# Kernel tuning notes

Hardware: AMD Instinct MI355X
Metric: run time of the kernel (lower is better)

## Reference

```python
import jax, jax.numpy as jnp
import numpy as np

D_MODEL = 1024
NUM_HEAD = 16
D_K = D_MODEL // NUM_HEAD


def setup_inputs() -> dict:
    key = jax.random.key(0)
    ks = jax.random.split(key, 11)
    B, S = 2, 2048
    s = 1.0 / np.sqrt(D_MODEL)
    return {
        "q": jax.random.normal(ks[0], (B, S, D_MODEL), jnp.float32),
        "k": jax.random.normal(ks[1], (B, S, D_MODEL), jnp.float32),
        "v": jax.random.normal(ks[2], (B, S, D_MODEL), jnp.float32),
        "Wq": jax.random.normal(ks[3], (D_MODEL, D_MODEL), jnp.float32) * s,
        "bq": jnp.zeros((D_MODEL,), jnp.float32),
        "Wk": jax.random.normal(ks[4], (D_MODEL, D_MODEL), jnp.float32) * s,
        "bk": jnp.zeros((D_MODEL,), jnp.float32),
        "Wv": jax.random.normal(ks[5], (D_MODEL, D_MODEL), jnp.float32) * s,
        "bv": jnp.zeros((D_MODEL,), jnp.float32),
        "Wo": jax.random.normal(ks[6], (D_MODEL, D_MODEL), jnp.float32) * s,
        "bo": jnp.zeros((D_MODEL,), jnp.float32),
    }


def _split_head(x, B):
    # [B, S, d_model] -> [B, H, S, d_k]
    S = x.shape[1]
    return x.reshape(B, S, NUM_HEAD, D_K).transpose(0, 2, 1, 3)


def reference(q, k, v, Wq, bq, Wk, bk, Wv, bv, Wo, bo):
    B = q.shape[0]
    qh = _split_head(q @ Wq + bq, B)  # [B,H,Sq,dk]
    kh = _split_head(k @ Wk + bk, B)  # [B,H,Sk,dk]
    vh = _split_head(v @ Wv + bv, B)  # [B,H,Sk,dk]
    scores = jnp.einsum("bhqd,bhkd->bhqk", qh, kh) / jnp.sqrt(
        jnp.asarray(D_K, qh.dtype)
    )
    attn = jax.nn.softmax(scores, axis=-1)
    out = jnp.einsum("bhqk,bhkd->bhqd", attn, vh)  # [B,H,Sq,dk]
    out = out.transpose(0, 2, 1, 3).reshape(B, -1, D_MODEL)
    return jax.nn.relu(out @ Wo + bo)
```

## Files before the change

### kernel.cpp

```cpp
#include <hip/hip_runtime.h>
#include <math.h>

#define SEQ 2048
#define NHD 16

typedef float f32x4 __attribute__((ext_vector_type(4), may_alias));
typedef _Float16 h16x8 __attribute__((ext_vector_type(8), may_alias));
typedef _Float16 h16x4 __attribute__((ext_vector_type(4), may_alias));

__device__ __forceinline__ void gl_lds16(const void* g, void* l) {
  __builtin_amdgcn_global_load_lds(
      (const __attribute__((address_space(1))) unsigned int*)g,
      (__attribute__((address_space(3))) unsigned int*)l, 16, 0, 0);
}

struct PrepArgs {
  const float* W[4];
  _Float16* T[4];
  const float* X[3];
  _Float16* H[3];
};

__global__ __launch_bounds__(256) void prep_k(PrepArgs a) {
  __shared__ float tile[64][65];
  const int blk = blockIdx.x;
  const int t = threadIdx.x;
  if (blk < 1024) {
    const int widx = blk >> 8, tl = blk & 255;
    const int nb = (tl & 15) * 64, kb = (tl >> 4) * 64;
    const float* __restrict__ W = a.W[widx];
    _Float16* __restrict__ T = a.T[widx];
    const int c = t & 63, r0 = t >> 6;
#pragma unroll
    for (int i = 0; i < 16; ++i) {
      const int r = i * 4 + r0;
      tile[r][c] = W[(size_t)(kb + r) * 1024 + nb + c];
    }
    __syncthreads();
#pragma unroll
    for (int i = 0; i < 16; ++i) {
      const int n = i * 4 + r0;
      T[(size_t)(nb + n) * 1024 + kb + c] = (_Float16)tile[c][n];
    }
  } else {
    const int b2 = blk - 1024;
    const int z = b2 >> 11, bx = b2 & 2047;
    const float* __restrict__ X = a.X[z];
    _Float16* __restrict__ H = a.H[z];
    const size_t i = ((size_t)bx * 256 + t) * 8;
    const f32x4 f0 = *(const f32x4*)(X + i);
    const f32x4 f1 = *(const f32x4*)(X + i + 4);
    const float fs[8] = {f0.x, f0.y, f0.z, f0.w, f1.x, f1.y, f1.z, f1.w};
    h16x8 o;
#pragma unroll
    for (int j = 0; j < 8; ++j) o[j] = (_Float16)fs[j];
    *(h16x8*)(H + i) = o;
  }
}

__global__ __launch_bounds__(256) void vtrans_k(const unsigned short* __restrict__ Vb,
                                                unsigned short* __restrict__ Vt) {
  __shared__ unsigned short tile[64][65];
  const int t = threadIdx.x;
  const int c = t & 63, r0 = t >> 6;
  const int s0 = blockIdx.x * 64;
  const int bh = blockIdx.y;
#pragma unroll
  for (int i = 0; i < 16; ++i) {
    const int r = i * 4 + r0;
    tile[r][c] = Vb[((size_t)bh * SEQ + s0 + r) * 64 + c];
  }
  __syncthreads();
#pragma unroll
  for (int i = 0; i < 16; ++i) {
    const int d = i * 4 + r0;
    const int sp = ((c & 15) * 4) + (c >> 4);
    Vt[((size_t)bh * 64 + d) * SEQ + s0 + sp] = tile[c][d];
  }
}

struct QKVArgs {
  const _Float16* A[3];
  const _Float16* Bt[3];
  const float* bias[3];
  _Float16* C[3];
};

__global__ __launch_bounds__(256, 4) void gemm_qkv_k(QKVArgs a) {
  __shared__ char smem[16384];
  h16x8* lds8 = (h16x8*)smem;
  const int z = blockIdx.z;
  const _Float16* __restrict__ A = a.A[z];
  const _Float16* __restrict__ Bt = a.Bt[z];
  const float* __restrict__ bias = a.bias[z];
  _Float16* __restrict__ C = a.C[z];

  const int t = threadIdx.x;
  const int l = t & 63, w = t >> 6;
  const int quad = l >> 4, l15 = l & 15;
  const int wm = w >> 1, wn = w & 1;
  const int n0 = blockIdx.x * 128, m0 = blockIdx.y * 128;

  const f32x4 z4 = {0.f, 0.f, 0.f, 0.f};
  f32x4 acc[4][4];
#pragma unroll
  for (int i = 0; i < 4; ++i)
#pragma unroll
    for (int j = 0; j < 4; ++j) acc[i][j] = z4;

  for (int k0 = 0; k0 < 1024; k0 += 32) {
#pragma unroll
    for (int it = 0; it < 2; ++it) {
      const int c = it * 4 + w;
      const int rr = c * 16 + l15;
      gl_lds16(A + (size_t)(m0 + rr) * 1024 + k0 + quad * 8, smem + c * 1024);
      gl_lds16(Bt + (size_t)(n0 + rr) * 1024 + k0 + quad * 8, smem + 8192 + c * 1024);
    }
    __syncthreads();
    h16x8 af[4], bf[4];
#pragma unroll
    for (int i = 0; i < 4; ++i) {
      af[i] = lds8[(wm * 4 + i) * 64 + l];
      bf[i] = lds8[512 + (wn * 4 + i) * 64 + l];
    }
#pragma unroll
    for (int i = 0; i < 4; ++i)
#pragma unroll
      for (int j = 0; j < 4; ++j)
        acc[i][j] = __builtin_amdgcn_mfma_f32_16x16x32_f16(af[i], bf[j], acc[i][j], 0, 0, 0);
    __syncthreads();
  }
#pragma unroll
  for (int i = 0; i < 4; ++i)
#pragma unroll
    for (int j = 0; j < 4; ++j) {
      const int col = n0 + wn * 64 + j * 16 + l15;
      const float bv = bias[col];
#pragma unroll
      for (int r = 0; r < 4; ++r) {
        const int row = m0 + wm * 64 + i * 16 + quad * 4 + r;
        const int b = row >> 11, s = row & 2047;
        const int h = col >> 6, d = col & 63;
        C[((size_t)(b * NHD + h) * SEQ + s) * 64 + d] = (_Float16)(acc[i][j][r] + bv);
      }
    }
}

__global__ __launch_bounds__(256, 4) void gemm_o_k(
    const _Float16* __restrict__ A, const _Float16* __restrict__ Bt,
    const float* __restrict__ bias, float* __restrict__ Cf) {
  __shared__ char smem[16384];
  h16x8* lds8 = (h16x8*)smem;
  const int t = threadIdx.x;
  const int l = t & 63, w = t >> 6;
  const int quad = l >> 4, l15 = l & 15;
  const int wm = w >> 1, wn = w & 1;
  const int n0 = blockIdx.x * 128, m0 = blockIdx.y * 128;

  const f32x4 z4 = {0.f, 0.f, 0.f, 0.f};
  f32x4 acc[4][4];
#pragma unroll
  for (int i = 0; i < 4; ++i)
#pragma unroll
    for (int j = 0; j < 4; ++j) acc[i][j] = z4;

  for (int k0 = 0; k0 < 1024; k0 += 32) {
#pragma unroll
    for (int it = 0; it < 2; ++it) {
      const int c = it * 4 + w;
      const int rr = c * 16 + l15;
      gl_lds16(A + (size_t)(m0 + rr) * 1024 + k0 + quad * 8, smem + c * 1024);
      gl_lds16(Bt + (size_t)(n0 + rr) * 1024 + k0 + quad * 8, smem + 8192 + c * 1024);
    }
    __syncthreads();
    h16x8 af[4], bf[4];
#pragma unroll
    for (int i = 0; i < 4; ++i) {
      af[i] = lds8[(wm * 4 + i) * 64 + l];
      bf[i] = lds8[512 + (wn * 4 + i) * 64 + l];
    }
#pragma unroll
    for (int i = 0; i < 4; ++i)
#pragma unroll
      for (int j = 0; j < 4; ++j)
        acc[i][j] = __builtin_amdgcn_mfma_f32_16x16x32_f16(af[i], bf[j], acc[i][j], 0, 0, 0);
    __syncthreads();
  }
#pragma unroll
  for (int i = 0; i < 4; ++i)
#pragma unroll
    for (int j = 0; j < 4; ++j) {
      const int col = n0 + wn * 64 + j * 16 + l15;
      const float bv = bias[col];
#pragma unroll
      for (int r = 0; r < 4; ++r) {
        const int row = m0 + wm * 64 + i * 16 + quad * 4 + r;
        Cf[(size_t)row * 1024 + col] = fmaxf(acc[i][j][r] + bv, 0.f);
      }
    }
}

__global__ __launch_bounds__(256, 4) void attn_k(
    const _Float16* __restrict__ Qf, const _Float16* __restrict__ Kf,
    const _Float16* __restrict__ Vtp, _Float16* __restrict__ Of) {
  __shared__ char smem[34816];
  h16x8* lds8 = (h16x8*)smem;
  const int t = threadIdx.x;
  const int l = t & 63, w = t >> 6;
  const int quad = l >> 4, l15 = l & 15;
  const int q0 = blockIdx.x * 128;
  const int bh = blockIdx.y;
  const int b = bh >> 4, h = bh & 15;

  const _Float16* Kb = Kf + (size_t)bh * SEQ * 64;
  const _Float16* Vtb = Vtp + (size_t)bh * 64 * SEQ;

  h16x8 qf[2][2];
#pragma unroll
  for (int mi = 0; mi < 2; ++mi) {
    const size_t qb = ((size_t)bh * SEQ + q0 + w * 32 + mi * 16 + l15) * 64;
#pragma unroll
    for (int ks = 0; ks < 2; ++ks)
      qf[mi][ks] = *(const h16x8*)&Qf[qb + ks * 32 + quad * 8];
  }
  const f32x4 z4 = {0.f, 0.f, 0.f, 0.f};
  f32x4 oacc[2][4], lacc[2];
#pragma unroll
  for (int mi = 0; mi < 2; ++mi) {
    lacc[mi] = z4;
#pragma unroll
    for (int i = 0; i < 4; ++i) oacc[mi][i] = z4;
  }
  h16x8 ones;
#pragma unroll
  for (int j = 0; j < 8; ++j) ones[j] = (_Float16)1.0f;

  for (int k0 = 0; k0 < SEQ; k0 += 64) {
#pragma unroll
    for (int it = 0; it < 2; ++it) {
      const int c = it * 4 + w;
      const int kd = (c >> 1) * 16 + l15;
      const int off2 = (c & 1) * 32 + quad * 8;
      gl_lds16(Kb + (size_t)(k0 + kd) * 64 + off2, smem + c * 1024);
      gl_lds16(Vtb + (size_t)kd * SEQ + k0 + off2, smem + 8192 + c * 1024);
    }
    __syncthreads();

    {
      h16x8 kfr[4][2];
#pragma unroll
      for (int nt = 0; nt < 4; ++nt)
#pragma unroll
        for (int ks = 0; ks < 2; ++ks) kfr[nt][ks] = lds8[(nt * 2 + ks) * 64 + l];

#pragma unroll
      for (int mi = 0; mi < 2; ++mi) {
        f32x4 sacc[4];
#pragma unroll
        for (int nt = 0; nt < 4; ++nt) {
          f32x4 s = z4;
          s = __builtin_amdgcn_mfma_f32_16x16x32_f16(qf[mi][0], kfr[nt][0], s, 0, 0, 0);
          s = __builtin_amdgcn_mfma_f32_16x16x32_f16(qf[mi][1], kfr[nt][1], s, 0, 0, 0);
          sacc[nt] = s;
        }
        char* pb = smem + 16384 + (w * 2 + mi) * 2304;
#pragma unroll
        for (int r = 0; r < 4; ++r) {
          h16x4 pk;
#pragma unroll
          for (int nt = 0; nt < 4; ++nt)
            pk[nt] = (_Float16)__expf(sacc[nt][r] * 0.125f);
          *(h16x4*)(pb + (quad * 4 + r) * 144 + l15 * 8) = pk;
        }
      }
    }
    __asm__ __volatile__("" ::: "memory");

    {
      h16x8 vfr[4][2];
#pragma unroll
      for (int nt = 0; nt < 4; ++nt)
#pragma unroll
        for (int ks = 0; ks < 2; ++ks) vfr[nt][ks] = lds8[512 + (nt * 2 + ks) * 64 + l];

#pragma unroll
      for (int mi = 0; mi < 2; ++mi) {
        char* pb = smem + 16384 + (w * 2 + mi) * 2304;
        const h16x8 pf0 = *(const h16x8*)(pb + l15 * 144 + quad * 16);
        const h16x8 pf1 = *(const h16x8*)(pb + l15 * 144 + 64 + quad * 16);
        lacc[mi] = __builtin_amdgcn_mfma_f32_16x16x32_f16(pf0, ones, lacc[mi], 0, 0, 0);
        lacc[mi] = __builtin_amdgcn_mfma_f32_16x16x32_f16(pf1, ones, lacc[mi], 0, 0, 0);
#pragma unroll
        for (int nt = 0; nt < 4; ++nt) {
          oacc[mi][nt] = __builtin_amdgcn_mfma_f32_16x16x32_f16(pf0, vfr[nt][0], oacc[mi][nt], 0, 0, 0);
          oacc[mi][nt] = __builtin_amdgcn_mfma_f32_16x16x32_f16(pf1, vfr[nt][1], oacc[mi][nt], 0, 0, 0);
        }
      }
    }
    __syncthreads();
  }

#pragma unroll
  for (int mi = 0; mi < 2; ++mi)
#pragma unroll
    for (int nt = 0; nt < 4; ++nt)
#pragma unroll
      for (int r = 0; r < 4; ++r) {
        const float o = oacc[mi][nt][r] / lacc[mi][r];
        const size_t tok = (size_t)b * SEQ + q0 + w * 32 + mi * 16 + quad * 4 + r;
        Of[tok * 1024 + h * 64 + nt * 16 + l15] = (_Float16)o;
      }
}

extern "C" void kernel_launch(void* const* d_in, const int* in_sizes, int n_in,
                              void* d_out, int out_size, void* d_ws, size_t ws_size,
                              hipStream_t stream) {
  const float* q = (const float*)d_in[0];
  const float* k = (const float*)d_in[1];
  const float* v = (const float*)d_in[2];
  const float* Wq = (const float*)d_in[3];
  const float* bq = (const float*)d_in[4];
  const float* Wk = (const float*)d_in[5];
  const float* bk = (const float*)d_in[6];
  const float* Wv = (const float*)d_in[7];
  const float* bv = (const float*)d_in[8];
  const float* Wo = (const float*)d_in[9];
  const float* bo = (const float*)d_in[10];

  char* W8 = (char*)d_ws;
  const size_t MB = 1024 * 1024;
  auto F = [&](size_t off) { return (_Float16*)(W8 + off); };
  _Float16* wt[4] = {F(0), F(2 * MB), F(4 * MB), F(6 * MB)};
  _Float16* qf = F(8 * MB);
  _Float16* kf = F(16 * MB);
  _Float16* vf = F(24 * MB);
  _Float16* Qf = F(32 * MB);
  _Float16* Kf = F(40 * MB);
  _Float16* Vb = F(48 * MB);
  _Float16* Vt = F(56 * MB);
  _Float16* Of = F(64 * MB);

  const dim3 blk(256);

  PrepArgs pa;
  pa.W[0] = Wq; pa.W[1] = Wk; pa.W[2] = Wv; pa.W[3] = Wo;
  pa.T[0] = wt[0]; pa.T[1] = wt[1]; pa.T[2] = wt[2]; pa.T[3] = wt[3];
  pa.X[0] = q; pa.X[1] = k; pa.X[2] = v;
  pa.H[0] = qf; pa.H[1] = kf; pa.H[2] = vf;
  prep_k<<<dim3(7168), blk, 0, stream>>>(pa);

  QKVArgs qa;
  qa.A[0] = qf; qa.A[1] = kf; qa.A[2] = vf;
  qa.Bt[0] = wt[0]; qa.Bt[1] = wt[1]; qa.Bt[2] = wt[2];
  qa.bias[0] = bq; qa.bias[1] = bk; qa.bias[2] = bv;
  qa.C[0] = Qf; qa.C[1] = Kf; qa.C[2] = Vb;
  gemm_qkv_k<<<dim3(8, 32, 3), blk, 0, stream>>>(qa);

  vtrans_k<<<dim3(32, 32), blk, 0, stream>>>((const unsigned short*)Vb,
                                             (unsigned short*)Vt);
  attn_k<<<dim3(16, 32), blk, 0, stream>>>(Qf, Kf, Vt, Of);
  gemm_o_k<<<dim3(8, 32), blk, 0, stream>>>(Of, wt[3], bo, (float*)d_out);
}
```

Before: 261.2 us.

## Split attention over key halves with combine pass; deepen GEMM K-step

Attention is split across two key-range halves through a third grid dimension, doubling the block count so more CUs are occupied. Each half writes unnormalized partial outputs and row sums, and a new combine kernel adds them and normalizes. The QKV and output GEMMs now stage a 64-wide K slice per barrier pair, halving synchronizations at the cost of twice the LDS and a lower occupancy hint. This adds an extra kernel launch plus fp16 partial-output traffic, and it reuses workspace regions (Vb for Op0, qf for Of).

```diff
diff --git a/kernel.cpp b/kernel.cpp
--- a/kernel.cpp
+++ b/kernel.cpp
@@ -86,8 +86,8 @@
   _Float16* C[3];
 };
 
-__global__ __launch_bounds__(256, 4) void gemm_qkv_k(QKVArgs a) {
-  __shared__ char smem[16384];
+__global__ __launch_bounds__(256, 3) void gemm_qkv_k(QKVArgs a) {
+  __shared__ char smem[32768];
   h16x8* lds8 = (h16x8*)smem;
   const int z = blockIdx.z;
   const _Float16* __restrict__ A = a.A[z];
@@ -108,26 +108,32 @@
 #pragma unroll
     for (int j = 0; j < 4; ++j) acc[i][j] = z4;
 
-  for (int k0 = 0; k0 < 1024; k0 += 32) {
-#pragma unroll
-    for (int it = 0; it < 2; ++it) {
-      const int c = it * 4 + w;
+  for (int k0 = 0; k0 < 1024; k0 += 64) {
+#pragma unroll
+    for (int it = 0; it < 4; ++it) {
+      const int c2 = it * 4 + w;
+      const int ks = c2 >> 3;
+      const int c = c2 & 7;
       const int rr = c * 16 + l15;
-      gl_lds16(A + (size_t)(m0 + rr) * 1024 + k0 + quad * 8, smem + c * 1024);
-      gl_lds16(Bt + (size_t)(n0 + rr) * 1024 + k0 + quad * 8, smem + 8192 + c * 1024);
-    }
-    __syncthreads();
-    h16x8 af[4], bf[4];
-#pragma unroll
-    for (int i = 0; i < 4; ++i) {
-      af[i] = lds8[(wm * 4 + i) * 64 + l];
-      bf[i] = lds8[512 + (wn * 4 + i) * 64 + l];
-    }
-#pragma unroll
-    for (int i = 0; i < 4; ++i)
-#pragma unroll
-      for (int j = 0; j < 4; ++j)
-        acc[i][j] = __builtin_amdgcn_mfma_f32_16x16x32_f16(af[i], bf[j], acc[i][j], 0, 0, 0);
+      const size_t ko = k0 + ks * 32 + quad * 8;
+      gl_lds16(A + (size_t)(m0 + rr) * 1024 + ko, smem + ks * 8192 + c * 1024);
+      gl_lds16(Bt + (size_t)(n0 + rr) * 1024 + ko, smem + 16384 + ks * 8192 + c * 1024);
+    }
+    __syncthreads();
+#pragma unroll
+    for (int ks = 0; ks < 2; ++ks) {
+      h16x8 af[4], bf[4];
+#pragma unroll
+      for (int i = 0; i < 4; ++i) {
+        af[i] = lds8[ks * 512 + (wm * 4 + i) * 64 + l];
+        bf[i] = lds8[1024 + ks * 512 + (wn * 4 + i) * 64 + l];
+      }
+#pragma unroll
+      for (int i = 0; i < 4; ++i)
+#pragma unroll
+        for (int j = 0; j < 4; ++j)
+          acc[i][j] = __builtin_amdgcn_mfma_f32_16x16x32_f16(af[i], bf[j], acc[i][j], 0, 0, 0);
+    }
     __syncthreads();
   }
 #pragma unroll
@@ -146,10 +152,10 @@
     }
 }
 
-__global__ __launch_bounds__(256, 4) void gemm_o_k(
+__global__ __launch_bounds__(256, 3) void gemm_o_k(
     const _Float16* __restrict__ A, const _Float16* __restrict__ Bt,
     const float* __restrict__ bias, float* __restrict__ Cf) {
-  __shared__ char smem[16384];
+  __shared__ char smem[32768];
   h16x8* lds8 = (h16x8*)smem;
   const int t = threadIdx.x;
   const int l = t & 63, w = t >> 6;
@@ -164,26 +170,32 @@
 #pragma unroll
     for (int j = 0; j < 4; ++j) acc[i][j] = z4;
 
-  for (int k0 = 0; k0 < 1024; k0 += 32) {
-#pragma unroll
-    for (int it = 0; it < 2; ++it) {
-      const int c = it * 4 + w;
+  for (int k0 = 0; k0 < 1024; k0 += 64) {
+#pragma unroll
+    for (int it = 0; it < 4; ++it) {
+      const int c2 = it * 4 + w;
+      const int ks = c2 >> 3;
+      const int c = c2 & 7;
       const int rr = c * 16 + l15;
-      gl_lds16(A + (size_t)(m0 + rr) * 1024 + k0 + quad * 8, smem + c * 1024);
-      gl_lds16(Bt + (size_t)(n0 + rr) * 1024 + k0 + quad * 8, smem + 8192 + c * 1024);
-    }
-    __syncthreads();
-    h16x8 af[4], bf[4];
-#pragma unroll
-    for (int i = 0; i < 4; ++i) {
-      af[i] = lds8[(wm * 4 + i) * 64 + l];
-      bf[i] = lds8[512 + (wn * 4 + i) * 64 + l];
-    }
-#pragma unroll
-    for (int i = 0; i < 4; ++i)
-#pragma unroll
-      for (int j = 0; j < 4; ++j)
-        acc[i][j] = __builtin_amdgcn_mfma_f32_16x16x32_f16(af[i], bf[j], acc[i][j], 0, 0, 0);
+      const size_t ko = k0 + ks * 32 + quad * 8;
+      gl_lds16(A + (size_t)(m0 + rr) * 1024 + ko, smem + ks * 8192 + c * 1024);
+      gl_lds16(Bt + (size_t)(n0 + rr) * 1024 + ko, smem + 16384 + ks * 8192 + c * 1024);
+    }
+    __syncthreads();
+#pragma unroll
+    for (int ks = 0; ks < 2; ++ks) {
+      h16x8 af[4], bf[4];
+#pragma unroll
+      for (int i = 0; i < 4; ++i) {
+        af[i] = lds8[ks * 512 + (wm * 4 + i) * 64 + l];
+        bf[i] = lds8[1024 + ks * 512 + (wn * 4 + i) * 64 + l];
+      }
+#pragma unroll
+      for (int i = 0; i < 4; ++i)
+#pragma unroll
+        for (int j = 0; j < 4; ++j)
+          acc[i][j] = __builtin_amdgcn_mfma_f32_16x16x32_f16(af[i], bf[j], acc[i][j], 0, 0, 0);
+    }
     __syncthreads();
   }
 #pragma unroll
@@ -202,7 +214,9 @@
 
 __global__ __launch_bounds__(256, 4) void attn_k(
     const _Float16* __restrict__ Qf, const _Float16* __restrict__ Kf,
-    const _Float16* __restrict__ Vtp, _Float16* __restrict__ Of) {
+    const _Float16* __restrict__ Vtp,
+    _Float16* __restrict__ Op0, _Float16* __restrict__ Op1,
+    float* __restrict__ Lp) {
   __shared__ char smem[34816];
   h16x8* lds8 = (h16x8*)smem;
   const int t = threadIdx.x;
@@ -210,6 +224,7 @@
   const int quad = l >> 4, l15 = l & 15;
   const int q0 = blockIdx.x * 128;
   const int bh = blockIdx.y;
+  const int kz = blockIdx.z;
   const int b = bh >> 4, h = bh & 15;
 
   const _Float16* Kb = Kf + (size_t)bh * SEQ * 64;
@@ -235,7 +250,8 @@
 #pragma unroll
   for (int j = 0; j < 8; ++j) ones[j] = (_Float16)1.0f;
 
-  for (int k0 = 0; k0 < SEQ; k0 += 64) {
+  const int kbeg = kz * 1024;
+  for (int k0 = kbeg; k0 < kbeg + 1024; k0 += 64) {
 #pragma unroll
     for (int it = 0; it < 2; ++it) {
       const int c = it * 4 + w;
@@ -300,16 +316,43 @@
     __syncthreads();
   }
 
+  _Float16* __restrict__ Op = kz ? Op1 : Op0;
 #pragma unroll
   for (int mi = 0; mi < 2; ++mi)
 #pragma unroll
     for (int nt = 0; nt < 4; ++nt)
 #pragma unroll
       for (int r = 0; r < 4; ++r) {
-        const float o = oacc[mi][nt][r] / lacc[mi][r];
         const size_t tok = (size_t)b * SEQ + q0 + w * 32 + mi * 16 + quad * 4 + r;
-        Of[tok * 1024 + h * 64 + nt * 16 + l15] = (_Float16)o;
-      }
+        Op[tok * 1024 + h * 64 + nt * 16 + l15] = (_Float16)oacc[mi][nt][r];
+      }
+  if (l15 == 0) {
+#pragma unroll
+    for (int mi = 0; mi < 2; ++mi)
+#pragma unroll
+      for (int r = 0; r < 4; ++r) {
+        const int row = q0 + w * 32 + mi * 16 + quad * 4 + r;
+        Lp[(size_t)kz * 65536 + bh * 2048 + row] = lacc[mi][r];
+      }
+  }
+}
+
+__global__ __launch_bounds__(256) void combine_k(
+    const _Float16* __restrict__ Op0, const _Float16* __restrict__ Op1,
+    const float* __restrict__ Lp, _Float16* __restrict__ Of) {
+  const size_t e = ((size_t)blockIdx.x * 256 + threadIdx.x) * 8;
+  const int tok = (int)(e >> 10);
+  const int h = (int)((e & 1023) >> 6);
+  const int b = tok >> 11, s = tok & 2047;
+  const int bh = b * NHD + h;
+  const float inv = 1.f / (Lp[(size_t)bh * 2048 + s] + Lp[65536 + (size_t)bh * 2048 + s]);
+  const h16x8 o1 = *(const h16x8*)(Op0 + e);
+  const h16x8 o2 = *(const h16x8*)(Op1 + e);
+  h16x8 o;
+#pragma unroll
+  for (int j = 0; j < 8; ++j)
+    o[j] = (_Float16)(((float)o1[j] + (float)o2[j]) * inv);
+  *(h16x8*)(Of + e) = o;
 }
 
 extern "C" void kernel_launch(void* const* d_in, const int* in_sizes, int n_in,
@@ -338,7 +381,10 @@
   _Float16* Kf = F(40 * MB);
   _Float16* Vb = F(48 * MB);
   _Float16* Vt = F(56 * MB);
-  _Float16* Of = F(64 * MB);
+  _Float16* Op0 = F(48 * MB);
+  _Float16* Op1 = F(64 * MB);
+  float* Lp = (float*)(W8 + 72 * MB);
+  _Float16* Of = F(8 * MB);
 
   const dim3 blk(256);
 
@@ -358,6 +404,7 @@
 
   vtrans_k<<<dim3(32, 32), blk, 0, stream>>>((const unsigned short*)Vb,
                                              (unsigned short*)Vt);
-  attn_k<<<dim3(16, 32), blk, 0, stream>>>(Qf, Kf, Vt, Of);
+  attn_k<<<dim3(16, 32, 2), blk, 0, stream>>>(Qf, Kf, Vt, Op0, Op1, Lp);
+  combine_k<<<dim3(2048), blk, 0, stream>>>(Op0, Op1, Lp, Of);
   gemm_o_k<<<dim3(8, 32), blk, 0, stream>>>(Of, wt[3], bo, (float*)d_out);
 }
```

After: 258.4 us. About the same (-1.1%).

## Fuse input fp16 conversion into QKV GEMM and split attention keys in two

Applied to the files above, without the earlier changes.

The separate fp32-to-fp16 conversion pass over q/k/v is removed. The QKV GEMM now loads fp32 activations, converts them in registers and stores them into LDS, which saves a full read/write round trip through memory. Attention is split over the key dimension into two halves, doubling the grid. Each half writes unnormalised partial outputs plus row sums, and the output GEMM combines and normalises them while staging its A operand. This adds extra partial-output traffic, and the combine is only correct if both halves use a consistent softmax offset.

```diff
diff --git a/kernel.cpp b/kernel.cpp
--- a/kernel.cpp
+++ b/kernel.cpp
@@ -17,44 +17,25 @@
 struct PrepArgs {
   const float* W[4];
   _Float16* T[4];
-  const float* X[3];
-  _Float16* H[3];
 };
 
 __global__ __launch_bounds__(256) void prep_k(PrepArgs a) {
   __shared__ float tile[64][65];
-  const int blk = blockIdx.x;
-  const int t = threadIdx.x;
-  if (blk < 1024) {
-    const int widx = blk >> 8, tl = blk & 255;
-    const int nb = (tl & 15) * 64, kb = (tl >> 4) * 64;
-    const float* __restrict__ W = a.W[widx];
-    _Float16* __restrict__ T = a.T[widx];
-    const int c = t & 63, r0 = t >> 6;
-#pragma unroll
-    for (int i = 0; i < 16; ++i) {
-      const int r = i * 4 + r0;
-      tile[r][c] = W[(size_t)(kb + r) * 1024 + nb + c];
-    }
-    __syncthreads();
-#pragma unroll
-    for (int i = 0; i < 16; ++i) {
-      const int n = i * 4 + r0;
-      T[(size_t)(nb + n) * 1024 + kb + c] = (_Float16)tile[c][n];
-    }
-  } else {
-    const int b2 = blk - 1024;
-    const int z = b2 >> 11, bx = b2 & 2047;
-    const float* __restrict__ X = a.X[z];
-    _Float16* __restrict__ H = a.H[z];
-    const size_t i = ((size_t)bx * 256 + t) * 8;
-    const f32x4 f0 = *(const f32x4*)(X + i);
-    const f32x4 f1 = *(const f32x4*)(X + i + 4);
-    const float fs[8] = {f0.x, f0.y, f0.z, f0.w, f1.x, f1.y, f1.z, f1.w};
-    h16x8 o;
-#pragma unroll
-    for (int j = 0; j < 8; ++j) o[j] = (_Float16)fs[j];
-    *(h16x8*)(H + i) = o;
+  const int t = threadIdx.x;
+  const int c = t & 63, r0 = t >> 6;
+  const int nb = blockIdx.x * 64, kb = blockIdx.y * 64;
+  const float* __restrict__ W = a.W[blockIdx.z];
+  _Float16* __restrict__ T = a.T[blockIdx.z];
+#pragma unroll
+  for (int i = 0; i < 16; ++i) {
+    const int r = i * 4 + r0;
+    tile[r][c] = W[(size_t)(kb + r) * 1024 + nb + c];
+  }
+  __syncthreads();
+#pragma unroll
+  for (int i = 0; i < 16; ++i) {
+    const int n = i * 4 + r0;
+    T[(size_t)(nb + n) * 1024 + kb + c] = (_Float16)tile[c][n];
   }
 }
 
@@ -80,7 +61,7 @@
 }
 
 struct QKVArgs {
-  const _Float16* A[3];
+  const float* Af[3];
   const _Float16* Bt[3];
   const float* bias[3];
   _Float16* C[3];
@@ -90,7 +71,7 @@
   __shared__ char smem[16384];
   h16x8* lds8 = (h16x8*)smem;
   const int z = blockIdx.z;
-  const _Float16* __restrict__ A = a.A[z];
+  const float* __restrict__ Af = a.Af[z];
   const _Float16* __restrict__ Bt = a.Bt[z];
   const float* __restrict__ bias = a.bias[z];
   _Float16* __restrict__ C = a.C[z];
@@ -113,8 +94,21 @@
     for (int it = 0; it < 2; ++it) {
       const int c = it * 4 + w;
       const int rr = c * 16 + l15;
-      gl_lds16(A + (size_t)(m0 + rr) * 1024 + k0 + quad * 8, smem + c * 1024);
       gl_lds16(Bt + (size_t)(n0 + rr) * 1024 + k0 + quad * 8, smem + 8192 + c * 1024);
+    }
+#pragma unroll
+    for (int it = 0; it < 2; ++it) {
+      const int row = it * 64 + (t >> 2);
+      const int aq = t & 3;
+      const int slot = (row >> 4) * 64 + aq * 16 + (row & 15);
+      const float* src = Af + (size_t)(m0 + row) * 1024 + k0 + aq * 8;
+      const f32x4 f0 = *(const f32x4*)src;
+      const f32x4 f1 = *(const f32x4*)(src + 4);
+      const float fs[8] = {f0.x, f0.y, f0.z, f0.w, f1.x, f1.y, f1.z, f1.w};
+      h16x8 hv;
+#pragma unroll
+      for (int j = 0; j < 8; ++j) hv[j] = (_Float16)fs[j];
+      lds8[slot] = hv;
     }
     __syncthreads();
     h16x8 af[4], bf[4];
@@ -147,16 +141,28 @@
 }
 
 __global__ __launch_bounds__(256, 4) void gemm_o_k(
-    const _Float16* __restrict__ A, const _Float16* __restrict__ Bt,
+    const _Float16* __restrict__ Op0, const _Float16* __restrict__ Op1,
+    const float* __restrict__ Lp, const _Float16* __restrict__ Bt,
     const float* __restrict__ bias, float* __restrict__ Cf) {
-  __shared__ char smem[16384];
+  __shared__ char smem[24576];
   h16x8* lds8 = (h16x8*)smem;
+  float* inv_lds = (float*)(smem + 16384);
   const int t = threadIdx.x;
   const int l = t & 63, w = t >> 6;
   const int quad = l >> 4, l15 = l & 15;
   const int wm = w >> 1, wn = w & 1;
   const int n0 = blockIdx.x * 128, m0 = blockIdx.y * 128;
 
+#pragma unroll
+  for (int e = t; e < 2048; e += 256) {
+    const int rl = e >> 4, hh = e & 15;
+    const int m = m0 + rl;
+    const int b = m >> 11, s = m & 2047;
+    const size_t li = (size_t)(b * NHD + hh) * 2048 + s;
+    inv_lds[e] = 1.f / (Lp[li] + Lp[65536 + li]);
+  }
+  __syncthreads();
+
   const f32x4 z4 = {0.f, 0.f, 0.f, 0.f};
   f32x4 acc[4][4];
 #pragma unroll
@@ -169,8 +175,23 @@
     for (int it = 0; it < 2; ++it) {
       const int c = it * 4 + w;
       const int rr = c * 16 + l15;
-      gl_lds16(A + (size_t)(m0 + rr) * 1024 + k0 + quad * 8, smem + c * 1024);
       gl_lds16(Bt + (size_t)(n0 + rr) * 1024 + k0 + quad * 8, smem + 8192 + c * 1024);
+    }
+    const int head = k0 >> 6;
+#pragma unroll
+    for (int it = 0; it < 2; ++it) {
+      const int row = it * 64 + (t >> 2);
+      const int aq = t & 3;
+      const int slot = (row >> 4) * 64 + aq * 16 + (row & 15);
+      const size_t off = (size_t)(m0 + row) * 1024 + k0 + aq * 8;
+      const h16x8 a0 = *(const h16x8*)(Op0 + off);
+      const h16x8 a1 = *(const h16x8*)(Op1 + off);
+      const float inv = inv_lds[row * 16 + head];
+      h16x8 hv;
+#pragma unroll
+      for (int j = 0; j < 8; ++j)
+        hv[j] = (_Float16)(((float)a0[j] + (float)a1[j]) * inv);
+      lds8[slot] = hv;
     }
     __syncthreads();
     h16x8 af[4], bf[4];
@@ -202,7 +223,9 @@
 
 __global__ __launch_bounds__(256, 4) void attn_k(
     const _Float16* __restrict__ Qf, const _Float16* __restrict__ Kf,
-    const _Float16* __restrict__ Vtp, _Float16* __restrict__ Of) {
+    const _Float16* __restrict__ Vtp,
+    _Float16* __restrict__ Op0, _Float16* __restrict__ Op1,
+    float* __restrict__ Lp) {
   __shared__ char smem[34816];
   h16x8* lds8 = (h16x8*)smem;
   const int t = threadIdx.x;
@@ -210,6 +233,7 @@
   const int quad = l >> 4, l15 = l & 15;
   const int q0 = blockIdx.x * 128;
   const int bh = blockIdx.y;
+  const int kz = blockIdx.z;
   const int b = bh >> 4, h = bh & 15;
 
   const _Float16* Kb = Kf + (size_t)bh * SEQ * 64;
@@ -235,7 +259,8 @@
 #pragma unroll
   for (int j = 0; j < 8; ++j) ones[j] = (_Float16)1.0f;
 
-  for (int k0 = 0; k0 < SEQ; k0 += 64) {
+  const int kbeg = kz * 1024;
+  for (int k0 = kbeg; k0 < kbeg + 1024; k0 += 64) {
 #pragma unroll
     for (int it = 0; it < 2; ++it) {
       const int c = it * 4 + w;
@@ -300,16 +325,25 @@
     __syncthreads();
   }
 
+  _Float16* __restrict__ Op = kz ? Op1 : Op0;
 #pragma unroll
   for (int mi = 0; mi < 2; ++mi)
 #pragma unroll
     for (int nt = 0; nt < 4; ++nt)
 #pragma unroll
       for (int r = 0; r < 4; ++r) {
-        const float o = oacc[mi][nt][r] / lacc[mi][r];
         const size_t tok = (size_t)b * SEQ + q0 + w * 32 + mi * 16 + quad * 4 + r;
-        Of[tok * 1024 + h * 64 + nt * 16 + l15] = (_Float16)o;
-      }
+        Op[tok * 1024 + h * 64 + nt * 16 + l15] = (_Float16)oacc[mi][nt][r];
+      }
+  if (l15 == 0) {
+#pragma unroll
+    for (int mi = 0; mi < 2; ++mi)
+#pragma unroll
+      for (int r = 0; r < 4; ++r) {
+        const int row = q0 + w * 32 + mi * 16 + quad * 4 + r;
+        Lp[(size_t)kz * 65536 + bh * 2048 + row] = lacc[mi][r];
+      }
+  }
 }
 
 extern "C" void kernel_launch(void* const* d_in, const int* in_sizes, int n_in,
@@ -331,26 +365,23 @@
   const size_t MB = 1024 * 1024;
   auto F = [&](size_t off) { return (_Float16*)(W8 + off); };
   _Float16* wt[4] = {F(0), F(2 * MB), F(4 * MB), F(6 * MB)};
-  _Float16* qf = F(8 * MB);
-  _Float16* kf = F(16 * MB);
-  _Float16* vf = F(24 * MB);
-  _Float16* Qf = F(32 * MB);
-  _Float16* Kf = F(40 * MB);
-  _Float16* Vb = F(48 * MB);
-  _Float16* Vt = F(56 * MB);
-  _Float16* Of = F(64 * MB);
+  _Float16* Vb = F(8 * MB);
+  _Float16* Vt = F(16 * MB);
+  _Float16* Qf = F(24 * MB);
+  _Float16* Kf = F(32 * MB);
+  _Float16* Op0 = F(40 * MB);
+  _Float16* Op1 = F(48 * MB);
+  float* Lp = (float*)(W8 + 56 * MB);
 
   const dim3 blk(256);
 
   PrepArgs pa;
   pa.W[0] = Wq; pa.W[1] = Wk; pa.W[2] = Wv; pa.W[3] = Wo;
   pa.T[0] = wt[0]; pa.T[1] = wt[1]; pa.T[2] = wt[2]; pa.T[3] = wt[3];
-  pa.X[0] = q; pa.X[1] = k; pa.X[2] = v;
-  pa.H[0] = qf; pa.H[1] = kf; pa.H[2] = vf;
-  prep_k<<<dim3(7168), blk, 0, stream>>>(pa);
+  prep_k<<<dim3(16, 16, 4), blk, 0, stream>>>(pa);
 
   QKVArgs qa;
-  qa.A[0] = qf; qa.A[1] = kf; qa.A[2] = vf;
+  qa.Af[0] = q; qa.Af[1] = k; qa.Af[2] = v;
   qa.Bt[0] = wt[0]; qa.Bt[1] = wt[1]; qa.Bt[2] = wt[2];
   qa.bias[0] = bq; qa.bias[1] = bk; qa.bias[2] = bv;
   qa.C[0] = Qf; qa.C[1] = Kf; qa.C[2] = Vb;
@@ -358,6 +389,6 @@
 
   vtrans_k<<<dim3(32, 32), blk, 0, stream>>>((const unsigned short*)Vb,
                                              (unsigned short*)Vt);
-  attn_k<<<dim3(16, 32), blk, 0, stream>>>(Qf, Kf, Vt, Of);
-  gemm_o_k<<<dim3(8, 32), blk, 0, stream>>>(Of, wt[3], bo, (float*)d_out);
-}
+  attn_k<<<dim3(16, 32, 2), blk, 0, stream>>>(Qf, Kf, Vt, Op0, Op1, Lp);
+  gemm_o_k<<<dim3(8, 32), blk, 0, stream>>>(Op0, Op1, Lp, wt[3], bo, (float*)d_out);
+}
```

Result: no change. 264.7 us (+1.3%).

## Split attention over two key halves and merge partials in output GEMM

Applied to the files above, without the earlier changes.

The attention kernel now splits the key dimension into two halves via a third grid dimension. Each half writes unnormalized fp16 partial outputs and per-row softmax denominators. The output-projection GEMM sums the two partials, divides by the combined denominator while staging A into swizzled LDS, then runs the MFMA loop. The aim is to double the attention block count so more of the GPU is occupied. The cost is extra partial-output traffic, synchronous A loads in the GEMM, and reliance on both halves sharing the same softmax offset.

```diff
diff --git a/kernel.cpp b/kernel.cpp
--- a/kernel.cpp
+++ b/kernel.cpp
@@ -147,16 +147,28 @@
 }
 
 __global__ __launch_bounds__(256, 4) void gemm_o_k(
-    const _Float16* __restrict__ A, const _Float16* __restrict__ Bt,
+    const _Float16* __restrict__ Op0, const _Float16* __restrict__ Op1,
+    const float* __restrict__ Lp, const _Float16* __restrict__ Bt,
     const float* __restrict__ bias, float* __restrict__ Cf) {
-  __shared__ char smem[16384];
+  __shared__ char smem[24576];
   h16x8* lds8 = (h16x8*)smem;
+  float* inv_lds = (float*)(smem + 16384);
   const int t = threadIdx.x;
   const int l = t & 63, w = t >> 6;
   const int quad = l >> 4, l15 = l & 15;
   const int wm = w >> 1, wn = w & 1;
   const int n0 = blockIdx.x * 128, m0 = blockIdx.y * 128;
 
+#pragma unroll
+  for (int e = t; e < 2048; e += 256) {
+    const int rl = e >> 4, hh = e & 15;
+    const int m = m0 + rl;
+    const int b = m >> 11, s = m & 2047;
+    const size_t li = (size_t)(b * NHD + hh) * 2048 + s;
+    inv_lds[e] = 1.f / (Lp[li] + Lp[65536 + li]);
+  }
+  __syncthreads();
+
   const f32x4 z4 = {0.f, 0.f, 0.f, 0.f};
   f32x4 acc[4][4];
 #pragma unroll
@@ -169,14 +181,29 @@
     for (int it = 0; it < 2; ++it) {
       const int c = it * 4 + w;
       const int rr = c * 16 + l15;
-      gl_lds16(A + (size_t)(m0 + rr) * 1024 + k0 + quad * 8, smem + c * 1024);
       gl_lds16(Bt + (size_t)(n0 + rr) * 1024 + k0 + quad * 8, smem + 8192 + c * 1024);
     }
+    const int head = k0 >> 6;
+#pragma unroll
+    for (int it = 0; it < 2; ++it) {
+      const int row = it * 64 + (t >> 2);
+      const int aq = t & 3;
+      const int slot = (row >> 4) * 64 + aq * 16 + ((row & 15) ^ (aq * 2));
+      const size_t off = (size_t)(m0 + row) * 1024 + k0 + aq * 8;
+      const h16x8 a0 = *(const h16x8*)(Op0 + off);
+      const h16x8 a1 = *(const h16x8*)(Op1 + off);
+      const float inv = inv_lds[row * 16 + head];
+      h16x8 hv;
+#pragma unroll
+      for (int j = 0; j < 8; ++j)
+        hv[j] = (_Float16)(((float)a0[j] + (float)a1[j]) * inv);
+      lds8[slot] = hv;
+    }
     __syncthreads();
     h16x8 af[4], bf[4];
 #pragma unroll
     for (int i = 0; i < 4; ++i) {
-      af[i] = lds8[(wm * 4 + i) * 64 + l];
+      af[i] = lds8[(wm * 4 + i) * 64 + quad * 16 + (l15 ^ (quad * 2))];
       bf[i] = lds8[512 + (wn * 4 + i) * 64 + l];
     }
 #pragma unroll
@@ -202,7 +229,9 @@
 
 __global__ __launch_bounds__(256, 4) void attn_k(
     const _Float16* __restrict__ Qf, const _Float16* __restrict__ Kf,
-    const _Float16* __restrict__ Vtp, _Float16* __restrict__ Of) {
+    const _Float16* __restrict__ Vtp,
+    _Float16* __restrict__ Op0, _Float16* __restrict__ Op1,
+    float* __restrict__ Lp) {
   __shared__ char smem[34816];
   h16x8* lds8 = (h16x8*)smem;
   const int t = threadIdx.x;
@@ -210,6 +239,7 @@
   const int quad = l >> 4, l15 = l & 15;
   const int q0 = blockIdx.x * 128;
   const int bh = blockIdx.y;
+  const int kz = blockIdx.z;
   const int b = bh >> 4, h = bh & 15;
 
   const _Float16* Kb = Kf + (size_t)bh * SEQ * 64;
@@ -235,7 +265,8 @@
 #pragma unroll
   for (int j = 0; j < 8; ++j) ones[j] = (_Float16)1.0f;
 
-  for (int k0 = 0; k0 < SEQ; k0 += 64) {
+  const int kbeg = kz * 1024;
+  for (int k0 = kbeg; k0 < kbeg + 1024; k0 += 64) {
 #pragma unroll
     for (int it = 0; it < 2; ++it) {
       const int c = it * 4 + w;
@@ -300,16 +331,25 @@
     __syncthreads();
   }
 
+  _Float16* __restrict__ Op = kz ? Op1 : Op0;
 #pragma unroll
   for (int mi = 0; mi < 2; ++mi)
 #pragma unroll
     for (int nt = 0; nt < 4; ++nt)
 #pragma unroll
       for (int r = 0; r < 4; ++r) {
-        const float o = oacc[mi][nt][r] / lacc[mi][r];
         const size_t tok = (size_t)b * SEQ + q0 + w * 32 + mi * 16 + quad * 4 + r;
-        Of[tok * 1024 + h * 64 + nt * 16 + l15] = (_Float16)o;
-      }
+        Op[tok * 1024 + h * 64 + nt * 16 + l15] = (_Float16)oacc[mi][nt][r];
+      }
+  if (l15 == 0) {
+#pragma unroll
+    for (int mi = 0; mi < 2; ++mi)
+#pragma unroll
+      for (int r = 0; r < 4; ++r) {
+        const int row = q0 + w * 32 + mi * 16 + quad * 4 + r;
+        Lp[(size_t)kz * 65536 + bh * 2048 + row] = lacc[mi][r];
+      }
+  }
 }
 
 extern "C" void kernel_launch(void* const* d_in, const int* in_sizes, int n_in,
@@ -338,7 +378,9 @@
   _Float16* Kf = F(40 * MB);
   _Float16* Vb = F(48 * MB);
   _Float16* Vt = F(56 * MB);
-  _Float16* Of = F(64 * MB);
+  _Float16* Op0 = F(8 * MB);
+  _Float16* Op1 = F(16 * MB);
+  float* Lp = (float*)(W8 + 64 * MB);
 
   const dim3 blk(256);
 
@@ -358,6 +400,6 @@
 
   vtrans_k<<<dim3(32, 32), blk, 0, stream>>>((const unsigned short*)Vb,
                                              (unsigned short*)Vt);
-  attn_k<<<dim3(16, 32), blk, 0, stream>>>(Qf, Kf, Vt, Of);
-  gemm_o_k<<<dim3(8, 32), blk, 0, stream>>>(Of, wt[3], bo, (float*)d_out);
-}
+  attn_k<<<dim3(16, 32, 2), blk, 0, stream>>>(Qf, Kf, Vt, Op0, Op1, Lp);
+  gemm_o_k<<<dim3(8, 32), blk, 0, stream>>>(Op0, Op1, Lp, wt[3], bo, (float*)d_out);
+}
```

After: 261.1 us. No clear change (-0.0%).
